# Kernel optimization log

Hardware: AMD Instinct MI355X
Metric: run time of the kernel (lower is better)

## Reference

```python
import jax, jax.numpy as jnp
import numpy as np
import jax.lax as lax

EPS_VAR = 1e-05  # hardcoded in original _get_statistics sqrt(var + 1e-05)


def _get_statistics(x):
    # x: (B, P, L). Cumulative NaN-aware mean/std along patch dim P.
    B, P, L = x.shape
    nan_mask = jnp.isnan(x)
    nan_counts = jnp.cumsum(nan_mask.sum(-1, keepdims=True).astype(x.dtype), axis=1)  # (B,P,1)
    counts = (jnp.arange(1, P + 1, dtype=x.dtype).reshape(1, P, 1)) * L - nan_counts   # (B,P,1)
    x0 = jnp.where(nan_mask, jnp.zeros_like(x), x)
    cumsum_x = jnp.cumsum(x0.sum(-1, keepdims=True), axis=1)          # nansum then cumsum
    mean = cumsum_x / counts
    cumsum_x2 = jnp.cumsum((x0 * x0).sum(-1, keepdims=True), axis=1)  # nansum of x^2
    var = (cumsum_x2 - 2.0 * mean * cumsum_x + counts * mean * mean) / counts
    std = jnp.sqrt(var + EPS_VAR)
    return mean, std


def _fill_nan_with_last_observed(x):
    # x: (B, P, L); forward-fill NaNs along last axis per (b,p) row.
    L = x.shape[-1]
    valid_mask = ~jnp.isnan(x)
    x_temp = jnp.where(valid_mask, x, jnp.zeros_like(x))
    seq_idx = jnp.arange(L, dtype=jnp.int32)
    valid_idx = jnp.where(valid_mask, seq_idx, jnp.int32(-1))
    last_valid = lax.cummax(valid_idx, axis=x.ndim - 1)
    return jnp.take_along_axis(x_temp, jnp.clip(last_valid, 0, None), axis=-1)


def setup_inputs() -> dict:
    key = jax.random.key(0)
    x = jax.random.normal(key, (128, 1024, 128), dtype=jnp.float32)
    return {"x": x}


def reference(x):
    # RevIN forward, mode='norm' (fresh cache). Original upcasts to float64;
    # we keep the input dtype (fp32) for kernel-comparison purposes.
    mean, std = _get_statistics(x)
    out = (x - mean) / std
    out = _fill_nan_with_last_observed(out)  # identity when no NaNs present
    return out.astype(jnp.float32)
```

## Files before the change

### kernel.cpp

```cpp
#include <hip/hip_runtime.h>
#include <math.h>

#define BB 128
#define PP 1024
#define LL 128
#define NROWS (BB * PP)
#define EPS_VAR 1e-5f
#define CHUNKS 8
#define CP (PP / CHUNKS)

typedef float vfloat4 __attribute__((ext_vector_type(4)));

__device__ __forceinline__ bool is_nan_bits(float f) {
    return (__float_as_uint(f) & 0x7fffffffu) > 0x7f800000u;
}

__global__ __launch_bounds__(256) void k_rowstats(const float* __restrict__ x,
                                                  float4* __restrict__ stats) {
    const int sl = threadIdx.x & 31;
    const int hw = (blockIdx.x * 256 + threadIdx.x) >> 5;
    const int row0 = hw * 2;
    const int row1 = row0 + 1;

    const float4 v0 = ((const float4*)(x + (size_t)row0 * LL))[sl];
    const float4 v1 = ((const float4*)(x + (size_t)row1 * LL))[sl];

    float s1a = 0.f, s2a = 0.f, ca = 0.f;
    float s1b = 0.f, s2b = 0.f, cb = 0.f;
    {
        const float fa[4] = {v0.x, v0.y, v0.z, v0.w};
        const float fb[4] = {v1.x, v1.y, v1.z, v1.w};
#pragma unroll
        for (int j = 0; j < 4; ++j) {
            const bool na = is_nan_bits(fa[j]);
            const float va = na ? 0.f : fa[j];
            s1a += va; s2a += va * va; ca += na ? 1.f : 0.f;
            const bool nb = is_nan_bits(fb[j]);
            const float vb = nb ? 0.f : fb[j];
            s1b += vb; s2b += vb * vb; cb += nb ? 1.f : 0.f;
        }
    }
#pragma unroll
    for (int off = 16; off >= 1; off >>= 1) {
        s1a += __shfl_xor(s1a, off);
        s2a += __shfl_xor(s2a, off);
        ca  += __shfl_xor(ca,  off);
        s1b += __shfl_xor(s1b, off);
        s2b += __shfl_xor(s2b, off);
        cb  += __shfl_xor(cb,  off);
    }
    if (sl == 0) {
        stats[row0] = make_float4(s1a, s2a, ca, 0.f);
        stats[row1] = make_float4(s1b, s2b, cb, 0.f);
    }
}

__global__ __launch_bounds__(256) void k_scan_norm(const float* __restrict__ x,
                                                   const float4* __restrict__ stats,
                                                   float* __restrict__ out) {
    __shared__ float2 ms_s[PP];
    __shared__ float w1[4], w2[4], wc[4];

    const int t     = threadIdx.x;
    const int lane  = t & 63;
    const int wav   = t >> 6;
    const int b     = blockIdx.x >> 3;
    const int chunk = blockIdx.x & (CHUNKS - 1);

    const size_t sbase = (size_t)b * PP + t * 4;
    float4 r[4];
#pragma unroll
    for (int j = 0; j < 4; ++j) r[j] = stats[sbase + j];

    float i1[4], i2[4], ic[4];
    i1[0] = r[0].x; i2[0] = r[0].y; ic[0] = r[0].z;
#pragma unroll
    for (int j = 1; j < 4; ++j) {
        i1[j] = i1[j - 1] + r[j].x;
        i2[j] = i2[j - 1] + r[j].y;
        ic[j] = ic[j - 1] + r[j].z;
    }
    const float t1 = i1[3], t2 = i2[3], tc = ic[3];

    float c1 = t1, c2 = t2, cc = tc;
#pragma unroll
    for (int off = 1; off < 64; off <<= 1) {
        const float a   = __shfl_up(c1, off);
        const float bb2 = __shfl_up(c2, off);
        const float cc2 = __shfl_up(cc, off);
        if (lane >= off) { c1 += a; c2 += bb2; cc += cc2; }
    }
    const float e1 = c1 - t1, e2 = c2 - t2, ec = cc - tc;

    if (lane == 63) { w1[wav] = c1; w2[wav] = c2; wc[wav] = cc; }
    __syncthreads();

    float p1 = 0.f, p2 = 0.f, pc = 0.f;
#pragma unroll
    for (int k = 0; k < 3; ++k) {
        if (wav > k) { p1 += w1[k]; p2 += w2[k]; pc += wc[k]; }
    }

    const float b1 = p1 + e1, b2 = p2 + e2, bc = pc + ec;
#pragma unroll
    for (int j = 0; j < 4; ++j) {
        const int p = t * 4 + j;
        const float cum1 = b1 + i1[j];
        const float cum2 = b2 + i2[j];
        const float cumc = bc + ic[j];
        const float cnt  = (float)(p + 1) * (float)LL - cumc;
        const float mean = cum1 / cnt;
        const float var  = cum2 / cnt - mean * mean;
        const float istd = 1.0f / sqrtf(var + EPS_VAR);
        ms_s[p] = make_float2(mean, istd);
    }
    __syncthreads();

    const int sl  = t & 31;
    const int hwl = t >> 5;
    const size_t bbase = (size_t)b * PP * LL;
    const int p0 = chunk * CP;

    for (int i = 0; i < CP; i += 16) {
        const int pa = p0 + i + hwl;
        const int pb = pa + 8;
        const size_t basea = bbase + (size_t)pa * LL;
        const size_t baseb = bbase + (size_t)pb * LL;

        const float4 v0 = ((const float4*)(x + basea))[sl];
        const float4 v1 = ((const float4*)(x + baseb))[sl];
        const float2 m0 = ms_s[pa];
        const float2 m1 = ms_s[pb];

        float4 y0, y1;
        y0.x = (v0.x - m0.x) * m0.y; y0.y = (v0.y - m0.x) * m0.y;
        y0.z = (v0.z - m0.x) * m0.y; y0.w = (v0.w - m0.x) * m0.y;
        y1.x = (v1.x - m1.x) * m1.y; y1.y = (v1.y - m1.x) * m1.y;
        y1.z = (v1.z - m1.x) * m1.y; y1.w = (v1.w - m1.x) * m1.y;

        const bool anynan = is_nan_bits(v0.x) | is_nan_bits(v0.y) | is_nan_bits(v0.z) |
                            is_nan_bits(v0.w) | is_nan_bits(v1.x) | is_nan_bits(v1.y) |
                            is_nan_bits(v1.z) | is_nan_bits(v1.w);

        if (__ballot(anynan) == 0ull) {
            vfloat4 w0 = {y0.x, y0.y, y0.z, y0.w};
            vfloat4 wv1 = {y1.x, y1.y, y1.z, y1.w};
            __builtin_nontemporal_store(w0,  &((vfloat4*)(out + basea))[sl]);
            __builtin_nontemporal_store(wv1, &((vfloat4*)(out + baseb))[sl]);
        } else {
            const size_t bases[2] = {basea, baseb};
            const float2 mm[2] = {m0, m1};
            const float4 vv[2] = {v0, v1};
            const float4 yy[2] = {y0, y1};
#pragma unroll
            for (int rr = 0; rr < 2; ++rr) {
                const float yf[4] = {yy[rr].x, yy[rr].y, yy[rr].z, yy[rr].w};
                const float vf[4] = {vv[rr].x, vv[rr].y, vv[rr].z, vv[rr].w};
                for (int j = 0; j < 4; ++j) {
                    const int l = sl * 4 + j;
                    if (!is_nan_bits(vf[j])) {
                        out[bases[rr] + l] = yf[j];
                    } else {
                        float res = 0.0f;
                        for (int k = l - 1; k >= 0; --k) {
                            const float xv = x[bases[rr] + k];
                            if (!is_nan_bits(xv)) {
                                res = (xv - mm[rr].x) * mm[rr].y;
                                break;
                            }
                        }
                        out[bases[rr] + l] = res;
                    }
                }
            }
        }
    }
}

extern "C" void kernel_launch(void* const* d_in, const int* in_sizes, int n_in,
                              void* d_out, int out_size, void* d_ws, size_t ws_size,
                              hipStream_t stream) {
    const float* x = (const float*)d_in[0];
    float* out = (float*)d_out;

    float4* stats = (float4*)d_ws;

    k_rowstats<<<NROWS / 16, 256, 0, stream>>>(x, stats);
    k_scan_norm<<<BB * CHUNKS, 256, 0, stream>>>(x, stats, out);
}
```

Baseline: 120.3 us.

## Prefetch chunk rows into registers before the stats scan and double chunk count

The number of chunks per batch doubles to 16, so each block normalizes 64 rows instead of 128 and the grid has twice as many blocks. Each block now issues all of its x loads into registers before the prefix scan of row statistics, so global-memory latency overlaps with the scan and its barriers instead of following them. The cost is more register pressure from the eight float4 buffers, plus every block redoing the full 1024-row stats scan, so that redundant scan work doubles.

```diff
diff --git a/kernel.cpp b/kernel.cpp
--- a/kernel.cpp
+++ b/kernel.cpp
@@ -6,7 +6,7 @@
 #define LL 128
 #define NROWS (BB * PP)
 #define EPS_VAR 1e-5f
-#define CHUNKS 8
+#define CHUNKS 16
 #define CP (PP / CHUNKS)
 
 typedef float vfloat4 __attribute__((ext_vector_type(4)));
@@ -64,13 +64,28 @@
     const int t     = threadIdx.x;
     const int lane  = t & 63;
     const int wav   = t >> 6;
-    const int b     = blockIdx.x >> 3;
+    const int b     = blockIdx.x >> 4;
     const int chunk = blockIdx.x & (CHUNKS - 1);
+    const int sl    = t & 31;
+    const int hwl   = t >> 5;
+    const size_t bbase = (size_t)b * PP * LL;
+    const int p0 = chunk * CP;
 
     const size_t sbase = (size_t)b * PP + t * 4;
     float4 r[4];
 #pragma unroll
     for (int j = 0; j < 4; ++j) r[j] = stats[sbase + j];
+
+    float4 v0[4], v1[4];
+    size_t basea[4], baseb[4];
+#pragma unroll
+    for (int i = 0; i < 4; ++i) {
+        const int pa = p0 + i * 16 + hwl;
+        basea[i] = bbase + (size_t)pa * LL;
+        baseb[i] = basea[i] + (size_t)8 * LL;
+        v0[i] = ((const float4*)(x + basea[i]))[sl];
+        v1[i] = ((const float4*)(x + baseb[i]))[sl];
+    }
 
     float i1[4], i2[4], ic[4];
     i1[0] = r[0].x; i2[0] = r[0].y; ic[0] = r[0].z;
@@ -116,41 +131,32 @@
     }
     __syncthreads();
 
-    const int sl  = t & 31;
-    const int hwl = t >> 5;
-    const size_t bbase = (size_t)b * PP * LL;
-    const int p0 = chunk * CP;
-
-    for (int i = 0; i < CP; i += 16) {
-        const int pa = p0 + i + hwl;
+#pragma unroll
+    for (int i = 0; i < 4; ++i) {
+        const int pa = p0 + i * 16 + hwl;
         const int pb = pa + 8;
-        const size_t basea = bbase + (size_t)pa * LL;
-        const size_t baseb = bbase + (size_t)pb * LL;
-
-        const float4 v0 = ((const float4*)(x + basea))[sl];
-        const float4 v1 = ((const float4*)(x + baseb))[sl];
         const float2 m0 = ms_s[pa];
         const float2 m1 = ms_s[pb];
 
         float4 y0, y1;
-        y0.x = (v0.x - m0.x) * m0.y; y0.y = (v0.y - m0.x) * m0.y;
-        y0.z = (v0.z - m0.x) * m0.y; y0.w = (v0.w - m0.x) * m0.y;
-        y1.x = (v1.x - m1.x) * m1.y; y1.y = (v1.y - m1.x) * m1.y;
-        y1.z = (v1.z - m1.x) * m1.y; y1.w = (v1.w - m1.x) * m1.y;
+        y0.x = (v0[i].x - m0.x) * m0.y; y0.y = (v0[i].y - m0.x) * m0.y;
+        y0.z = (v0[i].z - m0.x) * m0.y; y0.w = (v0[i].w - m0.x) * m0.y;
+        y1.x = (v1[i].x - m1.x) * m1.y; y1.y = (v1[i].y - m1.x) * m1.y;
+        y1.z = (v1[i].z - m1.x) * m1.y; y1.w = (v1[i].w - m1.x) * m1.y;
 
-        const bool anynan = is_nan_bits(v0.x) | is_nan_bits(v0.y) | is_nan_bits(v0.z) |
-                            is_nan_bits(v0.w) | is_nan_bits(v1.x) | is_nan_bits(v1.y) |
-                            is_nan_bits(v1.z) | is_nan_bits(v1.w);
+        const bool anynan = is_nan_bits(v0[i].x) | is_nan_bits(v0[i].y) | is_nan_bits(v0[i].z) |
+                            is_nan_bits(v0[i].w) | is_nan_bits(v1[i].x) | is_nan_bits(v1[i].y) |
+                            is_nan_bits(v1[i].z) | is_nan_bits(v1[i].w);
 
         if (__ballot(anynan) == 0ull) {
-            vfloat4 w0 = {y0.x, y0.y, y0.z, y0.w};
+            vfloat4 w0  = {y0.x, y0.y, y0.z, y0.w};
             vfloat4 wv1 = {y1.x, y1.y, y1.z, y1.w};
-            __builtin_nontemporal_store(w0,  &((vfloat4*)(out + basea))[sl]);
-            __builtin_nontemporal_store(wv1, &((vfloat4*)(out + baseb))[sl]);
+            __builtin_nontemporal_store(w0,  &((vfloat4*)(out + basea[i]))[sl]);
+            __builtin_nontemporal_store(wv1, &((vfloat4*)(out + baseb[i]))[sl]);
         } else {
-            const size_t bases[2] = {basea, baseb};
+            const size_t bases[2] = {basea[i], baseb[i]};
             const float2 mm[2] = {m0, m1};
-            const float4 vv[2] = {v0, v1};
+            const float4 vv[2] = {v0[i], v1[i]};
             const float4 yy[2] = {y0, y1};
 #pragma unroll
             for (int rr = 0; rr < 2; ++rr) {
```

Measured after the change: 121.0 us. Within noise of the previous version (+0.6%).

## Fuse row-stats and scan-normalize into one cooperative kernel holding x in registers

Applied to the files above, without the earlier changes.

Merges the two kernels into a single cooperative-launch kernel. Each block loads its 128 rows of x into registers, computes the row statistics, does a grid-wide sync, then runs the scan and normalizes from the registers. This removes the second read of x from memory and one kernel launch. In exchange it needs all 1024 blocks to be co-resident, which is why launch bounds are set to 4 blocks per CU, and the grid barrier plus high register use can limit latency hiding. If the cooperative launch fails, it falls back to the original two kernels.

```diff
diff --git a/kernel.cpp b/kernel.cpp
--- a/kernel.cpp
+++ b/kernel.cpp
@@ -1,4 +1,5 @@
 #include <hip/hip_runtime.h>
+#include <hip/hip_cooperative_groups.h>
 #include <math.h>
 
 #define BB 128
@@ -9,63 +10,73 @@
 #define CHUNKS 8
 #define CP (PP / CHUNKS)
 
+namespace cg = cooperative_groups;
+
 typedef float vfloat4 __attribute__((ext_vector_type(4)));
 
 __device__ __forceinline__ bool is_nan_bits(float f) {
     return (__float_as_uint(f) & 0x7fffffffu) > 0x7f800000u;
 }
 
-__global__ __launch_bounds__(256) void k_rowstats(const float* __restrict__ x,
-                                                  float4* __restrict__ stats) {
-    const int sl = threadIdx.x & 31;
-    const int hw = (blockIdx.x * 256 + threadIdx.x) >> 5;
-    const int row0 = hw * 2;
-    const int row1 = row0 + 1;
-
-    const float4 v0 = ((const float4*)(x + (size_t)row0 * LL))[sl];
-    const float4 v1 = ((const float4*)(x + (size_t)row1 * LL))[sl];
-
-    float s1a = 0.f, s2a = 0.f, ca = 0.f;
-    float s1b = 0.f, s2b = 0.f, cb = 0.f;
-    {
-        const float fa[4] = {v0.x, v0.y, v0.z, v0.w};
-        const float fb[4] = {v1.x, v1.y, v1.z, v1.w};
-#pragma unroll
-        for (int j = 0; j < 4; ++j) {
-            const bool na = is_nan_bits(fa[j]);
-            const float va = na ? 0.f : fa[j];
-            s1a += va; s2a += va * va; ca += na ? 1.f : 0.f;
-            const bool nb = is_nan_bits(fb[j]);
-            const float vb = nb ? 0.f : fb[j];
-            s1b += vb; s2b += vb * vb; cb += nb ? 1.f : 0.f;
-        }
-    }
-#pragma unroll
-    for (int off = 16; off >= 1; off >>= 1) {
-        s1a += __shfl_xor(s1a, off);
-        s2a += __shfl_xor(s2a, off);
-        ca  += __shfl_xor(ca,  off);
-        s1b += __shfl_xor(s1b, off);
-        s2b += __shfl_xor(s2b, off);
-        cb  += __shfl_xor(cb,  off);
-    }
-    if (sl == 0) {
-        stats[row0] = make_float4(s1a, s2a, ca, 0.f);
-        stats[row1] = make_float4(s1b, s2b, cb, 0.f);
-    }
-}
-
-__global__ __launch_bounds__(256) void k_scan_norm(const float* __restrict__ x,
-                                                   const float4* __restrict__ stats,
-                                                   float* __restrict__ out) {
+__global__ __launch_bounds__(256, 4) void k_fused(const float* __restrict__ x,
+                                                  float4* __restrict__ stats,
+                                                  float* __restrict__ out) {
     __shared__ float2 ms_s[PP];
     __shared__ float w1[4], w2[4], wc[4];
 
     const int t     = threadIdx.x;
+    const int sl    = t & 31;
+    const int hwl   = t >> 5;
     const int lane  = t & 63;
     const int wav   = t >> 6;
     const int b     = blockIdx.x >> 3;
     const int chunk = blockIdx.x & (CHUNKS - 1);
+    const int p0    = chunk * CP;
+    const size_t bbase = (size_t)b * (PP * LL);
+
+    float4 v0[8], v1[8];
+#pragma unroll
+    for (int i = 0; i < 8; ++i) {
+        const int pa = p0 + i * 16 + hwl;
+        const size_t basea = bbase + (size_t)pa * LL;
+        v0[i] = ((const float4*)(x + basea))[sl];
+        v1[i] = ((const float4*)(x + basea + 8 * LL))[sl];
+    }
+
+#pragma unroll
+    for (int i = 0; i < 8; ++i) {
+        float s1a = 0.f, s2a = 0.f, ca = 0.f;
+        float s1b = 0.f, s2b = 0.f, cb = 0.f;
+        {
+            const float fa[4] = {v0[i].x, v0[i].y, v0[i].z, v0[i].w};
+            const float fb[4] = {v1[i].x, v1[i].y, v1[i].z, v1[i].w};
+#pragma unroll
+            for (int j = 0; j < 4; ++j) {
+                const bool na = is_nan_bits(fa[j]);
+                const float va = na ? 0.f : fa[j];
+                s1a += va; s2a += va * va; ca += na ? 1.f : 0.f;
+                const bool nb = is_nan_bits(fb[j]);
+                const float vb = nb ? 0.f : fb[j];
+                s1b += vb; s2b += vb * vb; cb += nb ? 1.f : 0.f;
+            }
+        }
+#pragma unroll
+        for (int off = 16; off >= 1; off >>= 1) {
+            s1a += __shfl_xor(s1a, off);
+            s2a += __shfl_xor(s2a, off);
+            ca  += __shfl_xor(ca,  off);
+            s1b += __shfl_xor(s1b, off);
+            s2b += __shfl_xor(s2b, off);
+            cb  += __shfl_xor(cb,  off);
+        }
+        if (sl == 0) {
+            const int pa = p0 + i * 16 + hwl;
+            stats[(size_t)b * PP + pa]     = make_float4(s1a, s2a, ca, 0.f);
+            stats[(size_t)b * PP + pa + 8] = make_float4(s1b, s2b, cb, 0.f);
+        }
+    }
+
+    cg::this_grid().sync();
 
     const size_t sbase = (size_t)b * PP + t * 4;
     float4 r[4];
@@ -116,41 +127,34 @@
     }
     __syncthreads();
 
-    const int sl  = t & 31;
-    const int hwl = t >> 5;
-    const size_t bbase = (size_t)b * PP * LL;
-    const int p0 = chunk * CP;
-
-    for (int i = 0; i < CP; i += 16) {
-        const int pa = p0 + i + hwl;
+#pragma unroll
+    for (int i = 0; i < 8; ++i) {
+        const int pa = p0 + i * 16 + hwl;
         const int pb = pa + 8;
         const size_t basea = bbase + (size_t)pa * LL;
-        const size_t baseb = bbase + (size_t)pb * LL;
-
-        const float4 v0 = ((const float4*)(x + basea))[sl];
-        const float4 v1 = ((const float4*)(x + baseb))[sl];
+        const size_t baseb = basea + 8 * LL;
         const float2 m0 = ms_s[pa];
         const float2 m1 = ms_s[pb];
 
         float4 y0, y1;
-        y0.x = (v0.x - m0.x) * m0.y; y0.y = (v0.y - m0.x) * m0.y;
-        y0.z = (v0.z - m0.x) * m0.y; y0.w = (v0.w - m0.x) * m0.y;
-        y1.x = (v1.x - m1.x) * m1.y; y1.y = (v1.y - m1.x) * m1.y;
-        y1.z = (v1.z - m1.x) * m1.y; y1.w = (v1.w - m1.x) * m1.y;
-
-        const bool anynan = is_nan_bits(v0.x) | is_nan_bits(v0.y) | is_nan_bits(v0.z) |
-                            is_nan_bits(v0.w) | is_nan_bits(v1.x) | is_nan_bits(v1.y) |
-                            is_nan_bits(v1.z) | is_nan_bits(v1.w);
+        y0.x = (v0[i].x - m0.x) * m0.y; y0.y = (v0[i].y - m0.x) * m0.y;
+        y0.z = (v0[i].z - m0.x) * m0.y; y0.w = (v0[i].w - m0.x) * m0.y;
+        y1.x = (v1[i].x - m1.x) * m1.y; y1.y = (v1[i].y - m1.x) * m1.y;
+        y1.z = (v1[i].z - m1.x) * m1.y; y1.w = (v1[i].w - m1.x) * m1.y;
+
+        const bool anynan = is_nan_bits(v0[i].x) | is_nan_bits(v0[i].y) | is_nan_bits(v0[i].z) |
+                            is_nan_bits(v0[i].w) | is_nan_bits(v1[i].x) | is_nan_bits(v1[i].y) |
+                            is_nan_bits(v1[i].z) | is_nan_bits(v1[i].w);
 
         if (__ballot(anynan) == 0ull) {
-            vfloat4 w0 = {y0.x, y0.y, y0.z, y0.w};
+            vfloat4 w0  = {y0.x, y0.y, y0.z, y0.w};
             vfloat4 wv1 = {y1.x, y1.y, y1.z, y1.w};
             __builtin_nontemporal_store(w0,  &((vfloat4*)(out + basea))[sl]);
             __builtin_nontemporal_store(wv1, &((vfloat4*)(out + baseb))[sl]);
         } else {
             const size_t bases[2] = {basea, baseb};
             const float2 mm[2] = {m0, m1};
-            const float4 vv[2] = {v0, v1};
+            const float4 vv[2] = {v0[i], v1[i]};
             const float4 yy[2] = {y0, y1};
 #pragma unroll
             for (int rr = 0; rr < 2; ++rr) {
@@ -177,14 +181,181 @@
     }
 }
 
+__global__ __launch_bounds__(256) void k_rowstats(const float* __restrict__ x,
+                                                  float4* __restrict__ stats) {
+    const int sl = threadIdx.x & 31;
+    const int hw = (blockIdx.x * 256 + threadIdx.x) >> 5;
+    const int row0 = hw * 2;
+    const int row1 = row0 + 1;
+
+    const float4 v0 = ((const float4*)(x + (size_t)row0 * LL))[sl];
+    const float4 v1 = ((const float4*)(x + (size_t)row1 * LL))[sl];
+
+    float s1a = 0.f, s2a = 0.f, ca = 0.f;
+    float s1b = 0.f, s2b = 0.f, cb = 0.f;
+    {
+        const float fa[4] = {v0.x, v0.y, v0.z, v0.w};
+        const float fb[4] = {v1.x, v1.y, v1.z, v1.w};
+#pragma unroll
+        for (int j = 0; j < 4; ++j) {
+            const bool na = is_nan_bits(fa[j]);
+            const float va = na ? 0.f : fa[j];
+            s1a += va; s2a += va * va; ca += na ? 1.f : 0.f;
+            const bool nb = is_nan_bits(fb[j]);
+            const float vb = nb ? 0.f : fb[j];
+            s1b += vb; s2b += vb * vb; cb += nb ? 1.f : 0.f;
+        }
+    }
+#pragma unroll
+    for (int off = 16; off >= 1; off >>= 1) {
+        s1a += __shfl_xor(s1a, off);
+        s2a += __shfl_xor(s2a, off);
+        ca  += __shfl_xor(ca,  off);
+        s1b += __shfl_xor(s1b, off);
+        s2b += __shfl_xor(s2b, off);
+        cb  += __shfl_xor(cb,  off);
+    }
+    if (sl == 0) {
+        stats[row0] = make_float4(s1a, s2a, ca, 0.f);
+        stats[row1] = make_float4(s1b, s2b, cb, 0.f);
+    }
+}
+
+__global__ __launch_bounds__(256) void k_scan_norm(const float* __restrict__ x,
+                                                   const float4* __restrict__ stats,
+                                                   float* __restrict__ out) {
+    __shared__ float2 ms_s[PP];
+    __shared__ float w1[4], w2[4], wc[4];
+
+    const int t     = threadIdx.x;
+    const int lane  = t & 63;
+    const int wav   = t >> 6;
+    const int b     = blockIdx.x >> 3;
+    const int chunk = blockIdx.x & (CHUNKS - 1);
+
+    const size_t sbase = (size_t)b * PP + t * 4;
+    float4 r[4];
+#pragma unroll
+    for (int j = 0; j < 4; ++j) r[j] = stats[sbase + j];
+
+    float i1[4], i2[4], ic[4];
+    i1[0] = r[0].x; i2[0] = r[0].y; ic[0] = r[0].z;
+#pragma unroll
+    for (int j = 1; j < 4; ++j) {
+        i1[j] = i1[j - 1] + r[j].x;
+        i2[j] = i2[j - 1] + r[j].y;
+        ic[j] = ic[j - 1] + r[j].z;
+    }
+    const float t1 = i1[3], t2 = i2[3], tc = ic[3];
+
+    float c1 = t1, c2 = t2, cc = tc;
+#pragma unroll
+    for (int off = 1; off < 64; off <<= 1) {
+        const float a   = __shfl_up(c1, off);
+        const float bb2 = __shfl_up(c2, off);
+        const float cc2 = __shfl_up(cc, off);
+        if (lane >= off) { c1 += a; c2 += bb2; cc += cc2; }
+    }
+    const float e1 = c1 - t1, e2 = c2 - t2, ec = cc - tc;
+
+    if (lane == 63) { w1[wav] = c1; w2[wav] = c2; wc[wav] = cc; }
+    __syncthreads();
+
+    float p1 = 0.f, p2 = 0.f, pc = 0.f;
+#pragma unroll
+    for (int k = 0; k < 3; ++k) {
+        if (wav > k) { p1 += w1[k]; p2 += w2[k]; pc += wc[k]; }
+    }
+
+    const float b1 = p1 + e1, b2 = p2 + e2, bc = pc + ec;
+#pragma unroll
+    for (int j = 0; j < 4; ++j) {
+        const int p = t * 4 + j;
+        const float cum1 = b1 + i1[j];
+        const float cum2 = b2 + i2[j];
+        const float cumc = bc + ic[j];
+        const float cnt  = (float)(p + 1) * (float)LL - cumc;
+        const float mean = cum1 / cnt;
+        const float var  = cum2 / cnt - mean * mean;
+        const float istd = 1.0f / sqrtf(var + EPS_VAR);
+        ms_s[p] = make_float2(mean, istd);
+    }
+    __syncthreads();
+
+    const int sl  = t & 31;
+    const int hwl = t >> 5;
+    const size_t bbase = (size_t)b * PP * LL;
+    const int p0 = chunk * CP;
+
+    for (int i = 0; i < CP; i += 16) {
+        const int pa = p0 + i + hwl;
+        const int pb = pa + 8;
+        const size_t basea = bbase + (size_t)pa * LL;
+        const size_t baseb = bbase + (size_t)pb * LL;
+
+        const float4 v0 = ((const float4*)(x + basea))[sl];
+        const float4 v1 = ((const float4*)(x + baseb))[sl];
+        const float2 m0 = ms_s[pa];
+        const float2 m1 = ms_s[pb];
+
+        float4 y0, y1;
+        y0.x = (v0.x - m0.x) * m0.y; y0.y = (v0.y - m0.x) * m0.y;
+        y0.z = (v0.z - m0.x) * m0.y; y0.w = (v0.w - m0.x) * m0.y;
+        y1.x = (v1.x - m1.x) * m1.y; y1.y = (v1.y - m1.x) * m1.y;
+        y1.z = (v1.z - m1.x) * m1.y; y1.w = (v1.w - m1.x) * m1.y;
+
+        const bool anynan = is_nan_bits(v0.x) | is_nan_bits(v0.y) | is_nan_bits(v0.z) |
+                            is_nan_bits(v0.w) | is_nan_bits(v1.x) | is_nan_bits(v1.y) |
+                            is_nan_bits(v1.z) | is_nan_bits(v1.w);
+
+        if (__ballot(anynan) == 0ull) {
+            vfloat4 w0  = {y0.x, y0.y, y0.z, y0.w};
+            vfloat4 wv1 = {y1.x, y1.y, y1.z, y1.w};
+            __builtin_nontemporal_store(w0,  &((vfloat4*)(out + basea))[sl]);
+            __builtin_nontemporal_store(wv1, &((vfloat4*)(out + baseb))[sl]);
+        } else {
+            const size_t bases[2] = {basea, baseb};
+            const float2 mm[2] = {m0, m1};
+            const float4 vv[2] = {v0, v1};
+            const float4 yy[2] = {y0, y1};
+#pragma unroll
+            for (int rr = 0; rr < 2; ++rr) {
+                const float yf[4] = {yy[rr].x, yy[rr].y, yy[rr].z, yy[rr].w};
+                const float vf[4] = {vv[rr].x, vv[rr].y, vv[rr].z, vv[rr].w};
+                for (int j = 0; j < 4; ++j) {
+                    const int l = sl * 4 + j;
+                    if (!is_nan_bits(vf[j])) {
+                        out[bases[rr] + l] = yf[j];
+                    } else {
+                        float res = 0.0f;
+                        for (int k = l - 1; k >= 0; --k) {
+                            const float xv = x[bases[rr] + k];
+                            if (!is_nan_bits(xv)) {
+                                res = (xv - mm[rr].x) * mm[rr].y;
+                                break;
+                            }
+                        }
+                        out[bases[rr] + l] = res;
+                    }
+                }
+            }
+        }
+    }
+}
+
 extern "C" void kernel_launch(void* const* d_in, const int* in_sizes, int n_in,
                               void* d_out, int out_size, void* d_ws, size_t ws_size,
                               hipStream_t stream) {
     const float* x = (const float*)d_in[0];
     float* out = (float*)d_out;
-
     float4* stats = (float4*)d_ws;
 
-    k_rowstats<<<NROWS / 16, 256, 0, stream>>>(x, stats);
-    k_scan_norm<<<BB * CHUNKS, 256, 0, stream>>>(x, stats, out);
-}
+    void* args[] = {(void*)&x, (void*)&stats, (void*)&out};
+    hipError_t err = hipLaunchCooperativeKernel((const void*)k_fused,
+                                                dim3(BB * CHUNKS), dim3(256),
+                                                args, 0, stream);
+    if (err != hipSuccess) {
+        k_rowstats<<<NROWS / 16, 256, 0, stream>>>(x, stats);
+        k_scan_norm<<<BB * CHUNKS, 256, 0, stream>>>(x, stats, out);
+    }
+}
```

After: 214.8 us. 78.5% more time.
